# Optimization experiments

Hardware: AMD Instinct MI355X
Metric: run time of the kernel (lower is better)

The kernel has to match this reference:

```python
import jax, jax.numpy as jnp
import numpy as np

N = 100000      # nodes
E = 1600000     # edges (avg degree 16)
D_IN, D_H, D_OUT = 100, 256, 47
EPS = 1e-5


def setup_inputs() -> dict:
    key = jax.random.key(0)
    ks = jax.random.split(key, 10)
    w = lambda k, s: jax.random.normal(k, s, jnp.float32) * 0.02
    return {
        "x": jax.random.normal(ks[0], (N, D_IN), jnp.float32),
        "edge_index": jax.random.randint(ks[1], (2, E), 0, N),
        # SAGEConv 0: lin_l (aggregated neighbors, has bias), lin_r (root, no bias)
        "wl0": w(ks[2], (D_IN, D_H)), "wr0": w(ks[3], (D_IN, D_H)), "b0": jnp.zeros((D_H,), jnp.float32),
        "g0": jnp.ones((D_H,), jnp.float32), "be0": jnp.zeros((D_H,), jnp.float32),
        # SAGEConv 1
        "wl1": w(ks[4], (D_H, D_H)), "wr1": w(ks[5], (D_H, D_H)), "b1": jnp.zeros((D_H,), jnp.float32),
        "g1": jnp.ones((D_H,), jnp.float32), "be1": jnp.zeros((D_H,), jnp.float32),
        # SAGEConv 2 (output)
        "wl2": w(ks[6], (D_H, D_OUT)), "wr2": w(ks[7], (D_H, D_OUT)), "b2": jnp.zeros((D_OUT,), jnp.float32),
    }


def _sage_conv(x, src, dst, wl, wr, b):
    # mean aggregation of source-node features onto destination nodes
    agg = jax.ops.segment_sum(x[src], dst, num_segments=N)          # [N, d_in]
    cnt = jax.ops.segment_sum(jnp.ones((src.shape[0],), x.dtype), dst, num_segments=N)
    mean = agg / jnp.maximum(cnt, 1.0)[:, None]                     # 0 in-degree -> 0
    return mean @ wl + x @ wr + b


def _bn(h, gamma, beta):
    m = h.mean(axis=0)
    v = h.var(axis=0)
    return (h - m) * jax.lax.rsqrt(v + EPS) * gamma + beta


def reference(x, edge_index, wl0, wr0, b0, g0, be0, wl1, wr1, b1, g1, be1, wl2, wr2, b2):
    src, dst = edge_index[0], edge_index[1]
    h = jax.nn.relu(_bn(_sage_conv(x, src, dst, wl0, wr0, b0), g0, be0))
    h = jax.nn.relu(_bn(_sage_conv(h, src, dst, wl1, wr1, b1), g1, be1))
    h = _sage_conv(h, src, dst, wl2, wr2, b2)
    return jax.nn.log_softmax(h, axis=1)
```

## Files before the change

kernel.cpp:

```cpp
#include <hip/hip_runtime.h>
#include <hip/hip_bf16.h>
#include <math.h>

#define DEVFN __device__ __forceinline__

typedef unsigned int uint32;
typedef unsigned long long uint64;
typedef unsigned short ushort_t;

using bf16x8 = __attribute__((ext_vector_type(8))) short;
using f32x4  = __attribute__((ext_vector_type(4))) float;

DEVFN float bf2f(ushort_t u) {
    union { uint32 i; float f; } v; v.i = ((uint32)u) << 16; return v.f;
}
DEVFN ushort_t f2bf(float f) {
    union { float f; uint32 i; } v; v.f = f;
    uint32 u = v.i;
    uint32 r = (u + 0x7FFFu + ((u >> 16) & 1u)) >> 16;
    return (ushort_t)r;
}

DEVFN void gload_lds16(const void* g, void* l) {
    __builtin_amdgcn_global_load_lds(
        (const __attribute__((address_space(1))) void*)g,
        (__attribute__((address_space(3))) void*)l, 16, 0, 0);
}

__global__ void k_cast_x(const float* __restrict__ x, ushort_t* __restrict__ xb, int N) {
    int total = N * 128;
    for (int i = blockIdx.x * blockDim.x + threadIdx.x; i < total; i += gridDim.x * blockDim.x) {
        int col = i & 127, row = i >> 7;
        float v = (col < 100) ? x[row * 100 + col] : 0.f;
        xb[i] = f2bf(v);
    }
}

DEVFN void cast_one(const float* __restrict__ w, ushort_t* __restrict__ wt,
                    int j, int K, int Nout, int Kp) {
    int k = j % Kp, n = j / Kp;
    float v = (k < K && n < Nout) ? w[k * Nout + n] : 0.f;
    wt[j] = f2bf(v);
}

__global__ void k_cast_wall(const float* __restrict__ wl0, const float* __restrict__ wr0,
                            const float* __restrict__ wl1, const float* __restrict__ wr1,
                            const float* __restrict__ wl2, const float* __restrict__ wr2,
                            ushort_t* __restrict__ wlt0, ushort_t* __restrict__ wrt0,
                            ushort_t* __restrict__ wlt1, ushort_t* __restrict__ wrt1,
                            ushort_t* __restrict__ wcat2) {
    const int total = 229376;
    for (int i = blockIdx.x * blockDim.x + threadIdx.x; i < total; i += gridDim.x * blockDim.x) {
        int j = i;
        if (j < 32768)        cast_one(wl0, wlt0, j, 100, 256, 128);
        else if (j < 65536)   cast_one(wr0, wrt0, j - 32768, 100, 256, 128);
        else if (j < 131072)  cast_one(wl1, wlt1, j - 65536, 256, 256, 256);
        else if (j < 196608)  cast_one(wr1, wrt1, j - 131072, 256, 256, 256);
        else if (j < 212992)  cast_one(wl2, wcat2, j - 196608, 256, 47, 256);
        else                  cast_one(wr2, wcat2 + 16384, j - 212992, 256, 47, 256);
    }
}

__global__ void k_bincount(const int* __restrict__ dst, int E, int CH, int nbins, int nblk,
                           int* __restrict__ binCnt) {
    __shared__ int scnt[128];
    int blk = blockIdx.x, tid = threadIdx.x;
    for (int b = tid; b < 128; b += 256) scnt[b] = 0;
    __syncthreads();
    int e0 = blk * CH, e1 = min(E, e0 + CH);
    for (int i = e0 + tid; i < e1; i += 256)
        atomicAdd(&scnt[dst[i] >> 10], 1);
    __syncthreads();
    for (int b = tid; b < nbins; b += 256) binCnt[b * nblk + blk] = scnt[b];
}

__global__ void k_blocksum(const int* __restrict__ v, int n, int* __restrict__ bsum) {
    __shared__ int s[1024];
    int i = blockIdx.x * 1024 + threadIdx.x;
    s[threadIdx.x] = (i < n) ? v[i] : 0;
    __syncthreads();
    for (int o = 512; o > 0; o >>= 1) {
        if (threadIdx.x < o) s[threadIdx.x] += s[threadIdx.x + o];
        __syncthreads();
    }
    if (threadIdx.x == 0) bsum[blockIdx.x] = s[0];
}

__global__ void k_scanb(int* __restrict__ bsum, int NB) {
    if (blockIdx.x == 0 && threadIdx.x == 0) {
        int acc = 0;
        for (int i = 0; i < NB; ++i) { int v = bsum[i]; bsum[i] = acc; acc += v; }
    }
}

__global__ void k_exscan(const int* __restrict__ v, const int* __restrict__ bsum,
                         int n, int* __restrict__ outOff) {
    __shared__ int s[1024];
    int t = threadIdx.x;
    int i = blockIdx.x * 1024 + t;
    int val = (i < n) ? v[i] : 0;
    s[t] = val;
    __syncthreads();
    for (int o = 1; o < 1024; o <<= 1) {
        int add = (t >= o) ? s[t - o] : 0;
        __syncthreads();
        s[t] += add;
        __syncthreads();
    }
    if (i < n) outOff[i] = s[t] - val + bsum[blockIdx.x];
}

__global__ void k_binscatter(const int* __restrict__ src, const int* __restrict__ dst,
                             int E, int CH, int nbins, int nblk,
                             const int* __restrict__ binOff, int* __restrict__ ebin) {
    __shared__ int scur[128];
    int blk = blockIdx.x, tid = threadIdx.x;
    for (int b = tid; b < nbins; b += 256) scur[b] = binOff[b * nblk + blk];
    __syncthreads();
    int e0 = blk * CH, e1 = min(E, e0 + CH);
    for (int i = e0 + tid; i < e1; i += 256) {
        int d = dst[i];
        int b = d >> 10;
        int pos = atomicAdd(&scur[b], 1);
        ebin[pos] = (src[i] << 10) | (d & 1023);
    }
}

__global__ void k_bincsr(const int* __restrict__ ebin, const int* __restrict__ binOff,
                         int E, int N, int nbins, int nblk,
                         int* __restrict__ offs, int* __restrict__ deg, int* __restrict__ csr) {
    __shared__ int sdeg[1024];
    __shared__ int scur[1024];
    int bin = blockIdx.x, t = threadIdx.x;
    int binStart = binOff[bin * nblk];
    int binEnd = (bin + 1 < nbins) ? binOff[(bin + 1) * nblk] : E;
    sdeg[t] = 0;
    __syncthreads();
    for (int i = binStart + t; i < binEnd; i += 1024)
        atomicAdd(&sdeg[ebin[i] & 1023], 1);
    __syncthreads();
    int v = sdeg[t];
    for (int o = 1; o < 1024; o <<= 1) {
        int add = (t >= o) ? sdeg[t - o] : 0;
        __syncthreads();
        sdeg[t] += add;
        __syncthreads();
    }
    int ex = sdeg[t] - v;
    int node = bin * 1024 + t;
    if (node < N) { offs[node] = binStart + ex; deg[node] = v; }
    scur[t] = ex;
    __syncthreads();
    for (int i = binStart + t; i < binEnd; i += 1024) {
        int e = ebin[i];
        int slot = atomicAdd(&scur[e & 1023], 1);
        csr[binStart + slot] = e >> 10;
    }
}

template <int D, int BATCH>
__global__ __launch_bounds__(256) void k_agg(
    const ushort_t* __restrict__ h, const int* __restrict__ offs,
    const int* __restrict__ deg, const int* __restrict__ csr,
    int N, ushort_t* __restrict__ mean) {
    constexpr int LPR = D / 8;
    constexpr int EPG = 64 / LPR;
    constexpr int STEP = BATCH * EPG;
    int wid = (blockIdx.x * blockDim.x + threadIdx.x) >> 6;
    int lane = threadIdx.x & 63;
    if (wid >= N) return;
    const int seg = lane % LPR, sub = lane / LPR;
    int off = offs[wid], cnt = deg[wid];
    float a[8] = {};
    const ushort_t* hp = h + seg * 8;
    if (cnt > 0) {
        int idx[BATCH];
#pragma unroll
        for (int u = 0; u < BATCH; ++u)
            idx[u] = csr[off + min(u * EPG + sub, cnt - 1)];
        for (int b = 0; b < cnt; b += STEP) {
            uint4 d[BATCH];
#pragma unroll
            for (int u = 0; u < BATCH; ++u)
                d[u] = *(const uint4*)(hp + (size_t)idx[u] * D);
            int nxt = b + STEP;
#pragma unroll
            for (int u = 0; u < BATCH; ++u)
                idx[u] = csr[off + min(nxt + u * EPG + sub, cnt - 1)];
#pragma unroll
            for (int u = 0; u < BATCH; ++u) {
                float w = (b + u * EPG + sub < cnt) ? 1.f : 0.f;
                uint32 dd[4] = {d[u].x, d[u].y, d[u].z, d[u].w};
#pragma unroll
                for (int p = 0; p < 4; ++p) {
                    a[2 * p]     += w * bf2f((ushort_t)(dd[p] & 0xffff));
                    a[2 * p + 1] += w * bf2f((ushort_t)(dd[p] >> 16));
                }
            }
        }
    }
#pragma unroll
    for (int o = LPR; o < 64; o <<= 1) {
#pragma unroll
        for (int k = 0; k < 8; ++k) a[k] += __shfl_xor(a[k], o);
    }
    if (sub == 0) {
        float inv = 1.f / fmaxf((float)cnt, 1.f);
        uint4 o4;
        o4.x = (uint32)f2bf(a[0] * inv) | ((uint32)f2bf(a[1] * inv) << 16);
        o4.y = (uint32)f2bf(a[2] * inv) | ((uint32)f2bf(a[3] * inv) << 16);
        o4.z = (uint32)f2bf(a[4] * inv) | ((uint32)f2bf(a[5] * inv) << 16);
        o4.w = (uint32)f2bf(a[6] * inv) | ((uint32)f2bf(a[7] * inv) << 16);
        *(uint4*)(mean + (size_t)wid * D + seg * 8) = o4;
    }
}

template <int BN, int WROWS, int WCOLS, int MODE>
__global__ __launch_bounds__(512) void k_gemm(
    const ushort_t* __restrict__ A1, const ushort_t* __restrict__ B1,
    const ushort_t* __restrict__ A2, const ushort_t* __restrict__ B2,
    int KP, const float* __restrict__ bias,
    ushort_t* __restrict__ out_bf, float* __restrict__ out_f,
    float* __restrict__ stats, int M) {
    constexpr int BM = 128, BK = 64;
    constexpr int WM = BM / WROWS, WN = BN / WCOLS;
    constexpr int M_REP = WM / 16, N_REP = WN / 16;
    constexpr int SIDES = (MODE == 0) ? 2 : 1;
    __shared__ ushort_t Alds[BM * BK];
    __shared__ ushort_t Blds[BN * BK];
    __shared__ float sstat[2][BN];
    const int tid = threadIdx.x, lane = tid & 63, wid = tid >> 6;
    const int wm = wid / WCOLS, wn = wid % WCOLS;
    const int row0 = blockIdx.x * BM;
    if (MODE == 0) {
        for (int i = tid; i < 2 * BN; i += 512) (&sstat[0][0])[i] = 0.f;
    }
    f32x4 acc[M_REP][N_REP] = {};
    for (int side = 0; side < SIDES; ++side) {
        const ushort_t* A = side ? A2 : A1;
        const ushort_t* B = side ? B2 : B1;
        for (int kt = 0; kt < KP; kt += BK) {
            __syncthreads();
#pragma unroll
            for (int i = tid; i < BM * BK / 8; i += 512) {
                int r = i >> 3, c = i & 7;
                int gr = row0 + r;
                if (gr >= M) gr = M - 1;
                gload_lds16(A + (size_t)gr * KP + kt + c * 8, Alds + i * 8);
            }
#pragma unroll
            for (int i = tid; i < BN * BK / 8; i += 512) {
                int r = i >> 3, c = i & 7;
                gload_lds16(B + (size_t)r * KP + kt + c * 8, Blds + i * 8);
            }
            __syncthreads();
            bf16x8 a[2][M_REP], b[2][N_REP];
#pragma unroll
            for (int kk = 0; kk < 2; ++kk) {
#pragma unroll
                for (int m = 0; m < M_REP; ++m)
                    a[kk][m] = *(const bf16x8*)&Alds[(wm * WM + m * 16 + (lane & 15)) * BK + kk * 32 + (lane >> 4) * 8];
#pragma unroll
                for (int n = 0; n < N_REP; ++n)
                    b[kk][n] = *(const bf16x8*)&Blds[(wn * WN + n * 16 + (lane & 15)) * BK + kk * 32 + (lane >> 4) * 8];
            }
#pragma unroll
            for (int kk = 0; kk < 2; ++kk)
#pragma unroll
                for (int m = 0; m < M_REP; ++m)
#pragma unroll
                    for (int n = 0; n < N_REP; ++n)
                        acc[m][n] = __builtin_amdgcn_mfma_f32_16x16x32_bf16(a[kk][m], b[kk][n], acc[m][n], 0, 0, 0);
        }
    }
#pragma unroll
    for (int n = 0; n < N_REP; ++n) {
        int lcol = wn * WN + n * 16 + (lane & 15);
        float s = 0.f, q = 0.f;
#pragma unroll
        for (int m = 0; m < M_REP; ++m) {
#pragma unroll
            for (int r = 0; r < 4; ++r) {
                int row = row0 + wm * WM + m * 16 + (lane >> 4) * 4 + r;
                float v = acc[m][n][r];
                if (row < M) {
                    if (MODE == 0) {
                        out_bf[(size_t)row * 256 + lcol] = f2bf(v);
                        s += v;
                        q += v * v;
                    } else {
                        if (lcol < 64) {
                            out_bf[(size_t)row * 64 + lcol] = f2bf(v);
                        } else {
                            int c = lcol - 64;
                            float bv = (c < 47) ? bias[c] : 0.f;
                            out_f[(size_t)row * 64 + c] = v + bv;
                        }
                    }
                }
            }
        }
        if (MODE == 0) {
            s += __shfl_xor(s, 16); s += __shfl_xor(s, 32);
            q += __shfl_xor(q, 16); q += __shfl_xor(q, 32);
            if (lane < 16) {
                atomicAdd(&sstat[0][lcol], s);
                atomicAdd(&sstat[1][lcol], q);
            }
        }
    }
    if (MODE == 0) {
        __syncthreads();
        for (int i = tid; i < BN; i += 512) {
            atomicAdd(&stats[i], sstat[0][i]);
            atomicAdd(&stats[256 + i], sstat[1][i]);
        }
    }
}

__global__ void k_bnrelu(const ushort_t* __restrict__ h, const float* __restrict__ stats,
                         const float* __restrict__ g, const float* __restrict__ be,
                         int M, ushort_t* __restrict__ out) {
    int t = threadIdx.x;
    int cg = (t & 31) * 8;
    float invM = 1.f / (float)M;
    float sc[8], sh[8];
#pragma unroll
    for (int u = 0; u < 8; ++u) {
        int c = cg + u;
        float mean = stats[c] * invM;
        float var = stats[256 + c] * invM - mean * mean;
        float s = g[c] * rsqrtf(var + 1e-5f);
        sc[u] = s;
        sh[u] = be[c] - mean * s;
    }
    for (int r = blockIdx.x * 8 + (t >> 5); r < M; r += gridDim.x * 8) {
        uint4 d = *(const uint4*)(h + (size_t)r * 256 + cg);
        uint32 dd[4] = {d.x, d.y, d.z, d.w};
        uint32 w[4];
#pragma unroll
        for (int p = 0; p < 4; ++p) {
            float lo = bf2f((ushort_t)(dd[p] & 0xffff)) * sc[2 * p] + sh[2 * p];
            float hi = bf2f((ushort_t)(dd[p] >> 16)) * sc[2 * p + 1] + sh[2 * p + 1];
            w[p] = (uint32)f2bf(fmaxf(lo, 0.f)) | ((uint32)f2bf(fmaxf(hi, 0.f)) << 16);
        }
        uint4 o = {w[0], w[1], w[2], w[3]};
        *(uint4*)(out + (size_t)r * 256 + cg) = o;
    }
}

__global__ void k_agg_lsm(const ushort_t* __restrict__ t2, const float* __restrict__ r2,
                          const int* __restrict__ offs, const int* __restrict__ deg,
                          const int* __restrict__ csr, int N, float* __restrict__ out) {
    constexpr int LPR = 8, EPG = 8, BATCH = 2, STEP = 16;
    int wid = (blockIdx.x * blockDim.x + threadIdx.x) >> 6;
    int lane = threadIdx.x & 63;
    if (wid >= N) return;
    const int seg = lane & 7, sub = lane >> 3;
    int off = offs[wid], cnt = deg[wid];
    float a[8] = {};
    const ushort_t* tp = t2 + seg * 8;
    if (cnt > 0) {
        int idx[BATCH];
#pragma unroll
        for (int u = 0; u < BATCH; ++u)
            idx[u] = csr[off + min(u * EPG + sub, cnt - 1)];
        for (int b = 0; b < cnt; b += STEP) {
            uint4 d[BATCH];
#pragma unroll
            for (int u = 0; u < BATCH; ++u)
                d[u] = *(const uint4*)(tp + (size_t)idx[u] * 64);
            int nxt = b + STEP;
#pragma unroll
            for (int u = 0; u < BATCH; ++u)
                idx[u] = csr[off + min(nxt + u * EPG + sub, cnt - 1)];
#pragma unroll
            for (int u = 0; u < BATCH; ++u) {
                float w = (b + u * EPG + sub < cnt) ? 1.f : 0.f;
                uint32 dd[4] = {d[u].x, d[u].y, d[u].z, d[u].w};
#pragma unroll
                for (int p = 0; p < 4; ++p) {
                    a[2 * p]     += w * bf2f((ushort_t)(dd[p] & 0xffff));
                    a[2 * p + 1] += w * bf2f((ushort_t)(dd[p] >> 16));
                }
            }
        }
    }
#pragma unroll
    for (int o = 8; o < 64; o <<= 1) {
#pragma unroll
        for (int k = 0; k < 8; ++k) a[k] += __shfl_xor(a[k], o);
    }
    if (sub == 0) {
        float inv = 1.f / fmaxf((float)cnt, 1.f);
        float v[8];
#pragma unroll
        for (int k = 0; k < 8; ++k) {
            int c = seg * 8 + k;
            v[k] = a[k] * inv + r2[(size_t)wid * 64 + c];
            if (c >= 47) v[k] = -1e30f;
        }
        float m = v[0];
#pragma unroll
        for (int k = 1; k < 8; ++k) m = fmaxf(m, v[k]);
#pragma unroll
        for (int o = 1; o < 8; o <<= 1) m = fmaxf(m, __shfl_xor(m, o));
        float s = 0.f;
#pragma unroll
        for (int k = 0; k < 8; ++k) s += expf(v[k] - m);
#pragma unroll
        for (int o = 1; o < 8; o <<= 1) s += __shfl_xor(s, o);
        float lse = m + logf(s);
#pragma unroll
        for (int k = 0; k < 8; ++k) {
            int c = seg * 8 + k;
            if (c < 47) out[(size_t)wid * 47 + c] = v[k] - lse;
        }
    }
}

extern "C" void kernel_launch(void* const* d_in, const int* in_sizes, int n_in,
                              void* d_out, int out_size, void* d_ws, size_t ws_size,
                              hipStream_t stream) {
    const float* x   = (const float*)d_in[0];
    const int*   ei  = (const int*)d_in[1];
    const float* wl0 = (const float*)d_in[2];
    const float* wr0 = (const float*)d_in[3];
    const float* g0  = (const float*)d_in[5];
    const float* be0 = (const float*)d_in[6];
    const float* wl1 = (const float*)d_in[7];
    const float* wr1 = (const float*)d_in[8];
    const float* g1  = (const float*)d_in[10];
    const float* be1 = (const float*)d_in[11];
    const float* wl2 = (const float*)d_in[12];
    const float* wr2 = (const float*)d_in[13];
    const float* b2  = (const float*)d_in[14];
    float* out = (float*)d_out;

    const int N = in_sizes[0] / 100;
    const int E = in_sizes[1] / 2;
    const int* src = ei;
    const int* dst = ei + E;

    char* p = (char*)d_ws;
    auto alloc = [&](size_t bytes) -> char* {
        char* r = p;
        p += (bytes + 255) & ~(size_t)255;
        return r;
    };
    ushort_t* xb   = (ushort_t*)alloc((size_t)N * 128 * 2);
    ushort_t* hbuf = (ushort_t*)alloc((size_t)N * 256 * 2);
    ushort_t* mean = (ushort_t*)alloc((size_t)N * 256 * 2);
    ushort_t* hpre = (ushort_t*)alloc((size_t)N * 256 * 2);
    int* deg  = (int*)alloc((size_t)N * 4);
    int* offs = (int*)alloc((size_t)N * 4);
    int* csr  = (int*)alloc((size_t)E * 4);
    int* ebin = (int*)alloc((size_t)E * 4);
    const int NBLK = 128;
    const int nbins = (N + 1023) >> 10;
    const int scanN = nbins * NBLK;
    int* binCnt = (int*)alloc((size_t)scanN * 4);
    int* binOff = (int*)alloc((size_t)scanN * 4);
    int* bsum = (int*)alloc(1024 * 4);
    float* stats0 = (float*)alloc(512 * 4);
    float* stats1 = (float*)alloc(512 * 4);
    ushort_t* wlt0 = (ushort_t*)alloc(256 * 128 * 2);
    ushort_t* wrt0 = (ushort_t*)alloc(256 * 128 * 2);
    ushort_t* wlt1 = (ushort_t*)alloc(256 * 256 * 2);
    ushort_t* wrt1 = (ushort_t*)alloc(256 * 256 * 2);
    ushort_t* wcat2 = (ushort_t*)alloc(128 * 256 * 2);
    if ((size_t)(p - (char*)d_ws) > ws_size) return;

    ushort_t* t2 = mean;
    float*    r2 = (float*)((char*)mean + (size_t)N * 64 * 2);

    hipMemsetAsync(stats0, 0, 512 * 4, stream);
    hipMemsetAsync(stats1, 0, 512 * 4, stream);

    k_cast_x<<<2048, 256, 0, stream>>>(x, xb, N);
    k_cast_wall<<<896, 256, 0, stream>>>(wl0, wr0, wl1, wr1, wl2, wr2,
                                         wlt0, wrt0, wlt1, wrt1, wcat2);

    const int CH = (E + NBLK - 1) / NBLK;
    k_bincount<<<NBLK, 256, 0, stream>>>(dst, E, CH, nbins, NBLK, binCnt);
    int NB2 = (scanN + 1023) / 1024;
    k_blocksum<<<NB2, 1024, 0, stream>>>(binCnt, scanN, bsum);
    k_scanb<<<1, 64, 0, stream>>>(bsum, NB2);
    k_exscan<<<NB2, 1024, 0, stream>>>(binCnt, bsum, scanN, binOff);
    k_binscatter<<<NBLK, 256, 0, stream>>>(src, dst, E, CH, nbins, NBLK, binOff, ebin);
    k_bincsr<<<nbins, 1024, 0, stream>>>(ebin, binOff, E, N, nbins, NBLK, offs, deg, csr);

    int aggBlocks = (N + 3) / 4;
    int gemmM = (N + 127) / 128;

    k_agg<128, 4><<<aggBlocks, 256, 0, stream>>>(xb, offs, deg, csr, N, mean);
    k_gemm<256, 2, 4, 0><<<gemmM, 512, 0, stream>>>(
        mean, wlt0, xb, wrt0, 128, nullptr, hpre, nullptr, stats0, N);
    k_bnrelu<<<2048, 256, 0, stream>>>(hpre, stats0, g0, be0, N, hbuf);

    k_agg<256, 8><<<aggBlocks, 256, 0, stream>>>(hbuf, offs, deg, csr, N, mean);
    k_gemm<256, 2, 4, 0><<<gemmM, 512, 0, stream>>>(
        mean, wlt1, hbuf, wrt1, 256, nullptr, hpre, nullptr, stats1, N);
    k_bnrelu<<<2048, 256, 0, stream>>>(hpre, stats1, g1, be1, N, hbuf);

    k_gemm<128, 2, 4, 1><<<gemmM, 512, 0, stream>>>(
        hbuf, wcat2, nullptr, nullptr, 256, b2, t2, r2, nullptr, N);
    k_agg_lsm<<<(N + 3) / 4, 256, 0, stream>>>(t2, r2, offs, deg, csr, N, out);
}
```

Measured before the change: 551.6 us.

## Pad per-node CSR to multiples of 16 with zero-row sentinel for branchless aggregation

The CSR build now pads each node's neighbour list to a multiple of 16 using a sentinel index N. That index points at an extra all-zero feature row added to each feature buffer. The aggregation kernels drop the per-edge bounds clamps and masks, load neighbour indices as int4/int2 vectors, and accumulate in packed float2 pairs. The aim is to cut index-load and per-edge masking overhead in the memory-bound gathers. In exchange, padded slots cost extra (cached) loads of the zero row, the CSR array grows, and extra memsets are needed.

New measurement: 562.2 us. About the same (+1.9%).

```diff
diff --git a/kernel.cpp b/kernel.cpp
--- a/kernel.cpp
+++ b/kernel.cpp
@@ -5,14 +5,17 @@
 #define DEVFN __device__ __forceinline__
 
 typedef unsigned int uint32;
-typedef unsigned long long uint64;
 typedef unsigned short ushort_t;
 
 using bf16x8 = __attribute__((ext_vector_type(8))) short;
 using f32x4  = __attribute__((ext_vector_type(4))) float;
+using f32x2  = __attribute__((ext_vector_type(2))) float;
 
 DEVFN float bf2f(ushort_t u) {
     union { uint32 i; float f; } v; v.i = ((uint32)u) << 16; return v.f;
+}
+DEVFN float asf(uint32 u) {
+    union { uint32 i; float f; } v; v.i = u; return v.f;
 }
 DEVFN ushort_t f2bf(float f) {
     union { float f; uint32 i; } v; v.f = f;
@@ -128,77 +131,77 @@
 
 __global__ void k_bincsr(const int* __restrict__ ebin, const int* __restrict__ binOff,
                          int E, int N, int nbins, int nblk,
-                         int* __restrict__ offs, int* __restrict__ deg, int* __restrict__ csr) {
+                         int* __restrict__ poffs, int* __restrict__ deg, int* __restrict__ csr2) {
     __shared__ int sdeg[1024];
     __shared__ int scur[1024];
     int bin = blockIdx.x, t = threadIdx.x;
     int binStart = binOff[bin * nblk];
     int binEnd = (bin + 1 < nbins) ? binOff[(bin + 1) * nblk] : E;
+    int pbase = ((binStart + 15) & ~15) + bin * 15376;
     sdeg[t] = 0;
     __syncthreads();
     for (int i = binStart + t; i < binEnd; i += 1024)
         atomicAdd(&sdeg[ebin[i] & 1023], 1);
     __syncthreads();
     int v = sdeg[t];
+    int pv = (v + 15) & ~15;
+    sdeg[t] = pv;
+    __syncthreads();
     for (int o = 1; o < 1024; o <<= 1) {
         int add = (t >= o) ? sdeg[t - o] : 0;
         __syncthreads();
         sdeg[t] += add;
         __syncthreads();
     }
-    int ex = sdeg[t] - v;
+    int pex = sdeg[t] - pv;
     int node = bin * 1024 + t;
-    if (node < N) { offs[node] = binStart + ex; deg[node] = v; }
-    scur[t] = ex;
+    if (node < N) { poffs[node] = pbase + pex; deg[node] = v; }
+    scur[t] = pex;
     __syncthreads();
     for (int i = binStart + t; i < binEnd; i += 1024) {
         int e = ebin[i];
         int slot = atomicAdd(&scur[e & 1023], 1);
-        csr[binStart + slot] = e >> 10;
-    }
-}
-
-template <int D, int BATCH>
+        csr2[pbase + slot] = e >> 10;
+    }
+    for (int j = v; j < pv; ++j) csr2[pbase + pex + j] = N;
+}
+
+template <int D>
 __global__ __launch_bounds__(256) void k_agg(
-    const ushort_t* __restrict__ h, const int* __restrict__ offs,
-    const int* __restrict__ deg, const int* __restrict__ csr,
+    const ushort_t* __restrict__ h, const int* __restrict__ poffs,
+    const int* __restrict__ deg, const int* __restrict__ csr2,
     int N, ushort_t* __restrict__ mean) {
     constexpr int LPR = D / 8;
     constexpr int EPG = 64 / LPR;
-    constexpr int STEP = BATCH * EPG;
+    constexpr int STEP = 4 * EPG;
     int wid = (blockIdx.x * blockDim.x + threadIdx.x) >> 6;
     int lane = threadIdx.x & 63;
     if (wid >= N) return;
     const int seg = lane % LPR, sub = lane / LPR;
-    int off = offs[wid], cnt = deg[wid];
-    float a[8] = {};
+    int off = poffs[wid], cnt = deg[wid];
+    int pcnt = (cnt + 15) & ~15;
+    f32x2 acc[4] = {};
     const ushort_t* hp = h + seg * 8;
-    if (cnt > 0) {
-        int idx[BATCH];
-#pragma unroll
-        for (int u = 0; u < BATCH; ++u)
-            idx[u] = csr[off + min(u * EPG + sub, cnt - 1)];
-        for (int b = 0; b < cnt; b += STEP) {
-            uint4 d[BATCH];
-#pragma unroll
-            for (int u = 0; u < BATCH; ++u)
-                d[u] = *(const uint4*)(hp + (size_t)idx[u] * D);
-            int nxt = b + STEP;
-#pragma unroll
-            for (int u = 0; u < BATCH; ++u)
-                idx[u] = csr[off + min(nxt + u * EPG + sub, cnt - 1)];
-#pragma unroll
-            for (int u = 0; u < BATCH; ++u) {
-                float w = (b + u * EPG + sub < cnt) ? 1.f : 0.f;
-                uint32 dd[4] = {d[u].x, d[u].y, d[u].z, d[u].w};
-#pragma unroll
-                for (int p = 0; p < 4; ++p) {
-                    a[2 * p]     += w * bf2f((ushort_t)(dd[p] & 0xffff));
-                    a[2 * p + 1] += w * bf2f((ushort_t)(dd[p] >> 16));
-                }
-            }
-        }
-    }
+    int4 idx = *(const int4*)(csr2 + off + sub * 4);
+    for (int b = 0; b < pcnt; b += STEP) {
+        uint4 d0 = *(const uint4*)(hp + (size_t)idx.x * D);
+        uint4 d1 = *(const uint4*)(hp + (size_t)idx.y * D);
+        uint4 d2 = *(const uint4*)(hp + (size_t)idx.z * D);
+        uint4 d3 = *(const uint4*)(hp + (size_t)idx.w * D);
+        int4 idxn = *(const int4*)(csr2 + off + b + STEP + sub * 4);
+        uint32 dd[16] = {d0.x, d0.y, d0.z, d0.w, d1.x, d1.y, d1.z, d1.w,
+                         d2.x, d2.y, d2.z, d2.w, d3.x, d3.y, d3.z, d3.w};
+#pragma unroll
+        for (int q = 0; q < 16; ++q) {
+            f32x2 tv;
+            tv.x = asf(dd[q] << 16);
+            tv.y = asf(dd[q] & 0xffff0000u);
+            acc[q & 3] += tv;
+        }
+        idx = idxn;
+    }
+    float a[8] = {acc[0].x, acc[0].y, acc[1].x, acc[1].y,
+                  acc[2].x, acc[2].y, acc[3].x, acc[3].y};
 #pragma unroll
     for (int o = LPR; o < 64; o <<= 1) {
 #pragma unroll
@@ -350,42 +353,33 @@
 }
 
 __global__ void k_agg_lsm(const ushort_t* __restrict__ t2, const float* __restrict__ r2,
-                          const int* __restrict__ offs, const int* __restrict__ deg,
-                          const int* __restrict__ csr, int N, float* __restrict__ out) {
-    constexpr int LPR = 8, EPG = 8, BATCH = 2, STEP = 16;
+                          const int* __restrict__ poffs, const int* __restrict__ deg,
+                          const int* __restrict__ csr2, int N, float* __restrict__ out) {
     int wid = (blockIdx.x * blockDim.x + threadIdx.x) >> 6;
     int lane = threadIdx.x & 63;
     if (wid >= N) return;
     const int seg = lane & 7, sub = lane >> 3;
-    int off = offs[wid], cnt = deg[wid];
-    float a[8] = {};
+    int off = poffs[wid], cnt = deg[wid];
+    int pcnt = (cnt + 15) & ~15;
+    f32x2 acc[4] = {};
     const ushort_t* tp = t2 + seg * 8;
-    if (cnt > 0) {
-        int idx[BATCH];
-#pragma unroll
-        for (int u = 0; u < BATCH; ++u)
-            idx[u] = csr[off + min(u * EPG + sub, cnt - 1)];
-        for (int b = 0; b < cnt; b += STEP) {
-            uint4 d[BATCH];
-#pragma unroll
-            for (int u = 0; u < BATCH; ++u)
-                d[u] = *(const uint4*)(tp + (size_t)idx[u] * 64);
-            int nxt = b + STEP;
-#pragma unroll
-            for (int u = 0; u < BATCH; ++u)
-                idx[u] = csr[off + min(nxt + u * EPG + sub, cnt - 1)];
-#pragma unroll
-            for (int u = 0; u < BATCH; ++u) {
-                float w = (b + u * EPG + sub < cnt) ? 1.f : 0.f;
-                uint32 dd[4] = {d[u].x, d[u].y, d[u].z, d[u].w};
-#pragma unroll
-                for (int p = 0; p < 4; ++p) {
-                    a[2 * p]     += w * bf2f((ushort_t)(dd[p] & 0xffff));
-                    a[2 * p + 1] += w * bf2f((ushort_t)(dd[p] >> 16));
-                }
-            }
-        }
-    }
+    int2 idx = *(const int2*)(csr2 + off + sub * 2);
+    for (int b = 0; b < pcnt; b += 16) {
+        uint4 d0 = *(const uint4*)(tp + (size_t)idx.x * 64);
+        uint4 d1 = *(const uint4*)(tp + (size_t)idx.y * 64);
+        int2 idxn = *(const int2*)(csr2 + off + b + 16 + sub * 2);
+        uint32 dd[8] = {d0.x, d0.y, d0.z, d0.w, d1.x, d1.y, d1.z, d1.w};
+#pragma unroll
+        for (int q = 0; q < 8; ++q) {
+            f32x2 tv;
+            tv.x = asf(dd[q] << 16);
+            tv.y = asf(dd[q] & 0xffff0000u);
+            acc[q & 3] += tv;
+        }
+        idx = idxn;
+    }
+    float a[8] = {acc[0].x, acc[0].y, acc[1].x, acc[1].y,
+                  acc[2].x, acc[2].y, acc[3].x, acc[3].y};
 #pragma unroll
     for (int o = 8; o < 64; o <<= 1) {
 #pragma unroll
@@ -448,17 +442,18 @@
         p += (bytes + 255) & ~(size_t)255;
         return r;
     };
-    ushort_t* xb   = (ushort_t*)alloc((size_t)N * 128 * 2);
-    ushort_t* hbuf = (ushort_t*)alloc((size_t)N * 256 * 2);
-    ushort_t* mean = (ushort_t*)alloc((size_t)N * 256 * 2);
-    ushort_t* hpre = (ushort_t*)alloc((size_t)N * 256 * 2);
-    int* deg  = (int*)alloc((size_t)N * 4);
-    int* offs = (int*)alloc((size_t)N * 4);
-    int* csr  = (int*)alloc((size_t)E * 4);
-    int* ebin = (int*)alloc((size_t)E * 4);
     const int NBLK = 128;
     const int nbins = (N + 1023) >> 10;
     const int scanN = nbins * NBLK;
+    const size_t csr2N = (size_t)E + (size_t)nbins * 15376 + 64;
+    ushort_t* xb   = (ushort_t*)alloc(((size_t)N + 1) * 128 * 2);
+    ushort_t* hbuf = (ushort_t*)alloc(((size_t)N + 1) * 256 * 2);
+    ushort_t* meanB = (ushort_t*)alloc(((size_t)N + 1) * 256 * 2);
+    ushort_t* hpre = (ushort_t*)alloc((size_t)N * 256 * 2);
+    int* deg   = (int*)alloc((size_t)N * 4);
+    int* poffs = (int*)alloc((size_t)N * 4);
+    int* csr2  = (int*)alloc(csr2N * 4);
+    int* ebin  = (int*)alloc((size_t)E * 4);
     int* binCnt = (int*)alloc((size_t)scanN * 4);
     int* binOff = (int*)alloc((size_t)scanN * 4);
     int* bsum = (int*)alloc(1024 * 4);
@@ -471,11 +466,13 @@
     ushort_t* wcat2 = (ushort_t*)alloc(128 * 256 * 2);
     if ((size_t)(p - (char*)d_ws) > ws_size) return;
 
-    ushort_t* t2 = mean;
-    float*    r2 = (float*)((char*)mean + (size_t)N * 64 * 2);
+    ushort_t* t2 = meanB;
+    float*    r2 = (float*)(meanB + ((size_t)N + 1) * 64);
 
     hipMemsetAsync(stats0, 0, 512 * 4, stream);
     hipMemsetAsync(stats1, 0, 512 * 4, stream);
+    hipMemsetAsync(xb + (size_t)N * 128, 0, 128 * 2, stream);
+    hipMemsetAsync(hbuf + (size_t)N * 256, 0, 256 * 2, stream);
 
     k_cast_x<<<2048, 256, 0, stream>>>(x, xb, N);
     k_cast_wall<<<896, 256, 0, stream>>>(wl0, wr0, wl1, wr1, wl2, wr2,
@@ -488,22 +485,23 @@
     k_scanb<<<1, 64, 0, stream>>>(bsum, NB2);
     k_exscan<<<NB2, 1024, 0, stream>>>(binCnt, bsum, scanN, binOff);
     k_binscatter<<<NBLK, 256, 0, stream>>>(src, dst, E, CH, nbins, NBLK, binOff, ebin);
-    k_bincsr<<<nbins, 1024, 0, stream>>>(ebin, binOff, E, N, nbins, NBLK, offs, deg, csr);
+    k_bincsr<<<nbins, 1024, 0, stream>>>(ebin, binOff, E, N, nbins, NBLK, poffs, deg, csr2);
 
     int aggBlocks = (N + 3) / 4;
     int gemmM = (N + 127) / 128;
 
-    k_agg<128, 4><<<aggBlocks, 256, 0, stream>>>(xb, offs, deg, csr, N, mean);
+    k_agg<128><<<aggBlocks, 256, 0, stream>>>(xb, poffs, deg, csr2, N, meanB);
     k_gemm<256, 2, 4, 0><<<gemmM, 512, 0, stream>>>(
-        mean, wlt0, xb, wrt0, 128, nullptr, hpre, nullptr, stats0, N);
+        meanB, wlt0, xb, wrt0, 128, nullptr, hpre, nullptr, stats0, N);
     k_bnrelu<<<2048, 256, 0, stream>>>(hpre, stats0, g0, be0, N, hbuf);
 
-    k_agg<256, 8><<<aggBlocks, 256, 0, stream>>>(hbuf, offs, deg, csr, N, mean);
+    k_agg<256><<<aggBlocks, 256, 0, stream>>>(hbuf, poffs, deg, csr2, N, meanB);
     k_gemm<256, 2, 4, 0><<<gemmM, 512, 0, stream>>>(
-        mean, wlt1, hbuf, wrt1, 256, nullptr, hpre, nullptr, stats1, N);
+        meanB, wlt1, hbuf, wrt1, 256, nullptr, hpre, nullptr, stats1, N);
     k_bnrelu<<<2048, 256, 0, stream>>>(hpre, stats1, g1, be1, N, hbuf);
 
+    hipMemsetAsync(t2 + (size_t)N * 64, 0, 64 * 2, stream);
     k_gemm<128, 2, 4, 1><<<gemmM, 512, 0, stream>>>(
         hbuf, wcat2, nullptr, nullptr, 256, b2, t2, r2, nullptr, N);
-    k_agg_lsm<<<(N + 3) / 4, 256, 0, stream>>>(t2, r2, offs, deg, csr, N, out);
-}
+    k_agg_lsm<<<(N + 3) / 4, 256, 0, stream>>>(t2, r2, poffs, deg, csr2, N, out);
+}
```
